# Performance work log

Hardware: AMD Instinct MI355X
Metric: run time of the kernel (lower is better)

Reference implementation:

```python
import jax, jax.numpy as jnp
import numpy as np

E = 32          # n_routed_experts / num_local_experts
H = 1024        # hidden_size
I = 512         # moe_intermediate_size
G = 8           # n_group
TKG = 4         # topk_group
TOPK = 8        # num_experts_per_tok
NSH = 2         # n_shared_experts
SCALE = 2.5     # routed_scaling_factor


def setup_inputs() -> dict:
    key = jax.random.key(0)
    ks = jax.random.split(key, 10)
    s = 0.02
    return {
        "hidden_states": jax.random.normal(ks[0], (2, 1024, H), jnp.float32),
        # router: linear weight [E, H] and e_score_correction_bias [E]
        "gate_w": jax.random.normal(ks[1], (E, H), jnp.float32) * s,
        "gate_bias": jax.random.normal(ks[2], (E,), jnp.float32) * s,
        # routed experts (stacked SwiGLU weights, torch Linear layout [out, in])
        "w_gate": jax.random.normal(ks[3], (E, I, H), jnp.float32) * s,
        "w_up": jax.random.normal(ks[4], (E, I, H), jnp.float32) * s,
        "w_down": jax.random.normal(ks[5], (E, H, I), jnp.float32) * s,
        # shared experts: one MLP with intermediate = I * NSH
        "sh_gate": jax.random.normal(ks[6], (I * NSH, H), jnp.float32) * s,
        "sh_up": jax.random.normal(ks[7], (I * NSH, H), jnp.float32) * s,
        "sh_down": jax.random.normal(ks[8], (H, I * NSH), jnp.float32) * s,
    }


def reference(hidden_states, gate_w, gate_bias, w_gate, w_up, w_down,
              sh_gate, sh_up, sh_down):
    B, S, Hd = hidden_states.shape
    h = hidden_states.reshape(-1, Hd)                      # [T, H]

    # ---- router (DeepseekV3TopkRouter + route_tokens_to_experts) ----
    logits = h.astype(jnp.float32) @ gate_w.T              # [T, E]
    scores = jax.nn.sigmoid(logits)
    sc = scores + gate_bias                                # scores_for_choice
    # group score = sum of top-2 expert scores within each group
    grp = sc.reshape(-1, G, E // G)                        # [T, G, E/G]
    group_scores = jax.lax.top_k(grp, 2)[0].sum(-1)        # [T, G]
    gidx = jax.lax.top_k(group_scores, TKG)[1]             # [T, TKG]
    gmask = jnp.sum(jax.nn.one_hot(gidx, G, dtype=sc.dtype), axis=1)  # [T, G]
    smask = jnp.repeat(gmask, E // G, axis=1)              # [T, E]
    masked = jnp.where(smask > 0, sc, jnp.zeros_like(sc))  # masked_fill(~mask, 0)
    tki = jax.lax.top_k(masked, TOPK)[1]                   # [T, TOPK]
    tkw = jnp.take_along_axis(scores, tki, axis=1)         # gather raw sigmoid scores
    tkw = tkw / (tkw.sum(-1, keepdims=True) + 1e-20)       # norm_topk_prob
    tkw = tkw * SCALE

    # ---- dispatch-compute-combine (experts_forward) ----
    # combine[t, e] = sum_k tkw[t, k] * [tki[t, k] == e]
    combine = (jax.nn.one_hot(tki, E, dtype=tkw.dtype) * tkw[..., None]).sum(1)  # [T, E]
    g = jax.nn.silu(jnp.einsum('th,eih->tei', h, w_gate))  # [T, E, I]
    u = jnp.einsum('th,eih->tei', h, w_up)                 # [T, E, I]
    routed = jnp.einsum('tei,ehi->th', g * u * combine[:, :, None], w_down)  # [T, H]

    # ---- shared experts ----
    sg = jax.nn.silu(h @ sh_gate.T)
    shared = (sg * (h @ sh_up.T)) @ sh_down.T              # [T, H]

    return (routed + shared).reshape(B, S, Hd)
```

## Files before the change

kernel.cpp:

```cpp
#include <hip/hip_runtime.h>
#include <hip/hip_bf16.h>
#include <cstdint>

#define E_ 32
#define H_ 1024
#define I_ 512
#define G_ 8
#define NSH_ 2
#define SCALE_ 2.5f
#define NROUTED (E_ * I_)
#define PADCAP (16384 + E_ * 128)

typedef unsigned short u16;
using bf16x8_t = __attribute__((ext_vector_type(8))) __bf16;
using f32x4_t  = __attribute__((ext_vector_type(4))) float;

__device__ __forceinline__ u16 f2bf(float x) {
  union { float f; uint32_t u; } v; v.f = x;
  uint32_t u = v.u;
  uint32_t r = (u + 0x7fffu + ((u >> 16) & 1u)) >> 16;
  return (u16)r;
}
__device__ __forceinline__ float bf2f(u16 x) {
  union { uint32_t u; float f; } v; v.u = ((uint32_t)x) << 16; return v.f;
}

__device__ __forceinline__ void load_lds16(const void* g, void* l) {
  __builtin_amdgcn_global_load_lds(
      (const __attribute__((address_space(1))) unsigned int*)g,
      (__attribute__((address_space(3))) unsigned int*)l,
      16, 0, 0);
}

#define OFF_BU   16777216L
#define OFF_BD   33554432L
#define OFF_BSHG 50331648L
#define OFF_BSHU 51380224L
#define OFF_BSHD 52428800L
#define WBF_TOT  53477376L

#define W4_WG  4194304L
#define W4_WU  8388608L
#define W4_WD  12582912L
#define W4_SHG 12845056L
#define W4_SHU 13107200L
#define W4_TOT 13369344L
__global__ void prep_kernel(const float* __restrict__ gw, float* __restrict__ gwT,
                            int* __restrict__ counts, int* __restrict__ cursor,
                            int* __restrict__ qheads,
                            int* __restrict__ tok_list, float* __restrict__ wt_list,
                            const float* __restrict__ wg, const float* __restrict__ wu,
                            const float* __restrict__ wd, const float* __restrict__ shg,
                            const float* __restrict__ shu, const float* __restrict__ shd,
                            u16* __restrict__ wbf) {
  long i0 = (long)blockIdx.x * blockDim.x + threadIdx.x;
  if (i0 < H_ * E_) {
    int k = (int)(i0 >> 5), e = (int)(i0 & 31);
    gwT[i0] = gw[(long)e * H_ + k];
  }
  if (i0 < PADCAP) { tok_list[i0] = 0; wt_list[i0] = 0.f; }
  if (i0 < E_) { counts[i0] = 0; cursor[i0] = 0; }
  if (i0 < 2) qheads[i0] = 0;

  long stride = (long)gridDim.x * blockDim.x;
  for (long i = i0; i < W4_TOT; i += stride) {
    const float* s; long off; long dofs;
    if (i < W4_WG)       { s = wg;  off = i;            dofs = off * 4; }
    else if (i < W4_WU)  { s = wu;  off = i - W4_WG;    dofs = OFF_BU + off * 4; }
    else if (i < W4_WD)  { s = wd;  off = i - W4_WU;    dofs = OFF_BD + off * 4; }
    else if (i < W4_SHG) { s = shg; off = i - W4_WD;    dofs = OFF_BSHG + off * 4; }
    else if (i < W4_SHU) { s = shu; off = i - W4_SHG;   dofs = OFF_BSHU + off * 4; }
    else                 { s = shd; off = i - W4_SHU;   dofs = OFF_BSHD + off * 4; }
    float4 v = ((const float4*)s)[off];
    ushort4 o;
    o.x = f2bf(v.x); o.y = f2bf(v.y); o.z = f2bf(v.z); o.w = f2bf(v.w);
    *(ushort4*)(wbf + dofs) = o;
  }
}

__global__ __launch_bounds__(256) void logits_kernel(
    const float* __restrict__ h, const float* __restrict__ gwT,
    float* __restrict__ lpart,
    u16* __restrict__ hbf, int T) {
  __shared__ float shh[64][128];
  __shared__ float shw[128][E_];
  const int tid = threadIdx.x;
  const int t0 = blockIdx.x * 64;
  const int k0 = blockIdx.y * 128;
  #pragma unroll
  for (int i = 0; i < 8; ++i) {
    int c = tid + 256 * i;
    int row = c >> 5, col = c & 31;
    float4 v = *(const float4*)(h + (size_t)(t0 + row) * H_ + k0 + col * 4);
    *(float4*)(&shh[row][col * 4]) = v;
    ushort4 o;
    o.x = f2bf(v.x); o.y = f2bf(v.y); o.z = f2bf(v.z); o.w = f2bf(v.w);
    *(ushort4*)(hbf + (size_t)(t0 + row) * H_ + k0 + col * 4) = o;
  }
  #pragma unroll
  for (int i = 0; i < 4; ++i) {
    int c = tid + 256 * i;
    int row = c >> 3, col = c & 7;
    *(float4*)(&shw[row][col * 4]) =
        *(const float4*)(gwT + (size_t)(k0 + row) * E_ + col * 4);
  }
  __syncthreads();
  const int e = tid & 31;
  const int tb = (tid >> 5) * 8;
  float acc[8] = {0.f, 0.f, 0.f, 0.f, 0.f, 0.f, 0.f, 0.f};
  #pragma unroll 4
  for (int k = 0; k < 128; ++k) {
    float wv = shw[k][e];
    #pragma unroll
    for (int j = 0; j < 8; ++j) acc[j] += shh[tb + j][k] * wv;
  }
  #pragma unroll
  for (int j = 0; j < 8; ++j)
    lpart[((size_t)blockIdx.y * T + (t0 + tb + j)) * E_ + e] = acc[j];
}

__global__ __launch_bounds__(256) void topk_kernel(
    const float* __restrict__ lpart, const float* __restrict__ gb,
    int* __restrict__ idx8, float* __restrict__ wt8, int* __restrict__ counts,
    int T) {
  const int tid = threadIdx.x;
  const int l = tid & 63, wid = tid >> 6;
  const int e = l & 31, half = l >> 5;
  const int t = blockIdx.x * 8 + wid * 2 + half;

  float lg = 0.f;
  #pragma unroll
  for (int s = 0; s < 8; ++s) lg += lpart[((size_t)s * T + t) * E_ + e];
  float score = 1.f / (1.f + __expf(-lg));
  float sc = score + gb[e];

  float x1 = __shfl_xor(sc, 1);
  float x2 = __shfl_xor(sc, 2);
  float x3 = __shfl_xor(sc, 3);
  float hi1 = fmaxf(sc, x1), lo1 = fminf(sc, x1);
  float hi2 = fmaxf(x2, x3), lo2 = fminf(x2, x3);
  float m1 = fmaxf(hi1, hi2);
  float m2 = (hi1 >= hi2) ? fmaxf(lo1, hi2) : fmaxf(lo2, hi1);
  float gs = m1 + m2;

  float ga[8];
  #pragma unroll
  for (int g = 0; g < 8; ++g) ga[g] = __shfl(gs, (half << 5) + g * 4);
  unsigned gm = 0;
  #pragma unroll
  for (int r = 0; r < 4; ++r) {
    float bv = -1e30f; int bi = 0;
    #pragma unroll
    for (int g = 0; g < 8; ++g)
      if (!((gm >> g) & 1u) && ga[g] > bv) { bv = ga[g]; bi = g; }
    gm |= 1u << bi;
  }
  float msk = ((gm >> (e >> 2)) & 1u) ? sc : 0.f;

  float wsum = 0.f, myw = 0.f;
  int myi = 0;
  #pragma unroll
  for (int r = 0; r < 8; ++r) {
    float av = msk; int ai = e;
    #pragma unroll
    for (int m = 16; m; m >>= 1) {
      float ov = __shfl_xor(av, m);
      int oi = __shfl_xor(ai, m);
      if (ov > av || (ov == av && oi < ai)) { av = ov; ai = oi; }
    }
    float wscore = __shfl(score, (half << 5) + ai);
    wsum += wscore;
    if (e == r) { myi = ai; myw = wscore; }
    if (e == ai) msk = 0.f;
  }
  float inv = SCALE_ / (wsum + 1e-20f);
  if (e < 8) {
    idx8[(size_t)t * 8 + e] = myi;
    wt8[(size_t)t * 8 + e] = myw * inv;
    atomicAdd(&counts[myi], 1);
  }
}

__global__ void fill_kernel(const int* __restrict__ idx8, const float* __restrict__ wt8,
                            const int* __restrict__ counts, int* __restrict__ cursor,
                            int* __restrict__ tok_list, float* __restrict__ wt_list,
                            int* __restrict__ pair_pos, int npair) {
  int i = blockIdx.x * blockDim.x + threadIdx.x;
  if (i >= npair) return;
  int e = idx8[i];
  int offz = 0;
  for (int k = 0; k < E_; ++k) {
    if (k == e) break;
    offz += ((counts[k] + 127) >> 7) << 7;
  }
  int p = atomicAdd(&cursor[e], 1);
  int slot = offz + p;
  tok_list[slot] = i >> 3;
  wt_list[slot] = wt8[i];
  pair_pos[i] = slot;
}

__global__ __launch_bounds__(256, 3) void p1_kernel(
    const u16* __restrict__ hbf,
    const u16* __restrict__ wbf,
    const int* __restrict__ counts,
    const int* __restrict__ tok_list, const float* __restrict__ wt_list,
    int* __restrict__ qheads,
    u16* __restrict__ gu,
    u16* __restrict__ gu_sh,
    int T) {
  __shared__ u16 lsA[3][128 * 32];
  __shared__ u16 lsB0[3][64 * 32];
  __shared__ u16 lsB1[3][64 * 32];
  __shared__ int s_tok[128];
  __shared__ float s_wt[128];
  __shared__ int s_off[E_], s_ntt[E_];
  __shared__ int s_tot, s_tile;

  const int tid = threadIdx.x;
  if (tid == 0) {
    int run = 0, tot = 0;
    for (int e = 0; e < E_; ++e) {
      s_off[e] = run;
      int nt = (counts[e] + 127) >> 7;
      s_ntt[e] = nt;
      run += nt << 7;
      tot += nt * 8;
    }
    s_tot = tot + (T / 128) * 16;
  }

  const int w = tid >> 6, l = tid & 63;
  const int wr = w >> 1, wc = w & 1;
  const int lr = l & 15, lh = l >> 4;
  const int rdblk = (lh ^ ((lr >> 1) & 3)) << 3;

  const int rA0 = tid >> 2,          cb0 = tid & 3, sc0 = cb0 ^ ((rA0 >> 1) & 3);
  const int rA1 = (tid + 256) >> 2,  sc1 = cb0 ^ ((rA1 >> 1) & 3);

  for (;;) {
    __syncthreads();
    if (tid == 0) s_tile = atomicAdd(&qheads[0], 1);
    __syncthreads();
    int q = s_tile;
    if (q >= s_tot) break;

    int z = 0, rem = q;
    for (; z < E_; ++z) { int t = s_ntt[z] * 8; if (rem < t) break; rem -= t; }
    const bool sh_e = (z == E_);
    int tt, nb;
    if (sh_e) { nb = rem >> 4; tt = rem & 15; }
    else      { int nt = s_ntt[z]; nb = rem / nt; tt = rem - nb * nt; }
    const int off = sh_e ? 0 : s_off[z];

    if (tid < 128) {
      if (sh_e) { s_tok[tid] = tt * 128 + tid; s_wt[tid] = 1.0f; }
      else {
        int slot = off + tt * 128 + tid;
        s_tok[tid] = tok_list[slot];
        s_wt[tid] = wt_list[slot];
      }
    }
    __syncthreads();

    const u16* Bg = sh_e ? (wbf + OFF_BSHG + (size_t)(nb * 64) * H_)
                         : (wbf + ((size_t)z * I_ + nb * 64) * H_);
    const u16* Bu = sh_e ? (wbf + OFF_BSHU + (size_t)(nb * 64) * H_)
                         : (wbf + OFF_BU + ((size_t)z * I_ + nb * 64) * H_);
    const u16* A0p = hbf + (size_t)s_tok[rA0] * H_ + sc0 * 8;
    const u16* A1p = hbf + (size_t)s_tok[rA1] * H_ + sc1 * 8;
    const u16* Bgp = Bg + (size_t)rA0 * H_ + sc0 * 8;
    const u16* Bup = Bu + (size_t)rA0 * H_ + sc0 * 8;

    f32x4_t acc0[4][2], acc1[4][2];
    #pragma unroll
    for (int m = 0; m < 4; ++m)
      #pragma unroll
      for (int n = 0; n < 2; ++n) {
        acc0[m][n] = (f32x4_t){0.f, 0.f, 0.f, 0.f};
        acc1[m][n] = (f32x4_t){0.f, 0.f, 0.f, 0.f};
      }

    auto stage = [&](int b, int ks) {
      int k0 = ks * 32;
      load_lds16(A0p + k0, (char*)&lsA[b][0] + tid * 16);
      load_lds16(A1p + k0, (char*)&lsA[b][0] + (tid + 256) * 16);
      load_lds16(Bgp + k0, (char*)&lsB0[b][0] + tid * 16);
      load_lds16(Bup + k0, (char*)&lsB1[b][0] + tid * 16);
    };
    auto compute = [&](int b) {
      bf16x8_t af[4], b0f[2], b1f[2];
      #pragma unroll
      for (int m = 0; m < 4; ++m)
        af[m] = *(const bf16x8_t*)(&lsA[b][0] + (wr * 64 + m * 16 + lr) * 32 + rdblk);
      #pragma unroll
      for (int n = 0; n < 2; ++n) {
        b0f[n] = *(const bf16x8_t*)(&lsB0[b][0] + (wc * 32 + n * 16 + lr) * 32 + rdblk);
        b1f[n] = *(const bf16x8_t*)(&lsB1[b][0] + (wc * 32 + n * 16 + lr) * 32 + rdblk);
      }
      #pragma unroll
      for (int m = 0; m < 4; ++m)
        #pragma unroll
        for (int n = 0; n < 2; ++n) {
          acc0[m][n] = __builtin_amdgcn_mfma_f32_16x16x32_bf16(af[m], b0f[n], acc0[m][n], 0, 0, 0);
          acc1[m][n] = __builtin_amdgcn_mfma_f32_16x16x32_bf16(af[m], b1f[n], acc1[m][n], 0, 0, 0);
        }
    };

    stage(0, 0);
    stage(1, 1);
    int b0 = 0, b1 = 1, b2 = 2;
    #pragma unroll 1
    for (int s = 0; s < 31; ++s) {
      asm volatile("s_waitcnt vmcnt(4)" ::: "memory");
      __builtin_amdgcn_s_barrier();
      compute(b0);
      if (s < 30) stage(b2, s + 2);
      int tb = b0; b0 = b1; b1 = b2; b2 = tb;
    }
    asm volatile("s_waitcnt vmcnt(0)" ::: "memory");
    __builtin_amdgcn_s_barrier();
    compute(b0);

    const int ldo = sh_e ? (I_ * NSH_) : I_;
    u16* outp = sh_e ? (gu_sh + (size_t)(tt * 128) * ldo + nb * 64)
                     : (gu + (size_t)(off + tt * 128) * ldo + nb * 64);
    #pragma unroll
    for (int m = 0; m < 4; ++m) {
      #pragma unroll
      for (int n = 0; n < 2; ++n) {
        int col = wc * 32 + n * 16 + lr;
        #pragma unroll
        for (int j = 0; j < 4; ++j) {
          int trow = wr * 64 + m * 16 + lh * 4 + j;
          float gv = acc0[m][n][j], uv = acc1[m][n][j];
          float sv = gv / (1.f + __expf(-gv));
          outp[(size_t)trow * ldo + col] = f2bf(sv * uv * s_wt[trow]);
        }
      }
    }
  }
}

__global__ __launch_bounds__(256, 3) void p2_kernel(
    const u16* __restrict__ gu, const u16* __restrict__ gu_sh,
    const u16* __restrict__ wbf,
    const int* __restrict__ counts,
    int* __restrict__ qheads,
    u16* __restrict__ part,
    u16* __restrict__ part_sh,
    int T) {
  __shared__ u16 lsA[3][128 * 32];
  __shared__ u16 lsB[3][128 * 32];
  __shared__ int s_off[E_], s_ntt[E_];
  __shared__ int s_tot, s_tile;

  const int tid = threadIdx.x;
  if (tid == 0) {
    int run = 0, tot = 0;
    for (int e = 0; e < E_; ++e) {
      s_off[e] = run;
      int nt = (counts[e] + 127) >> 7;
      s_ntt[e] = nt;
      run += nt << 7;
      tot += nt * 8;
    }
    s_tot = tot + (T / 128) * 8;
  }

  const int w = tid >> 6, l = tid & 63;
  const int wr = w >> 1, wc = w & 1;
  const int lr = l & 15, lh = l >> 4;
  const int rdblk = (lh ^ ((lr >> 1) & 3)) << 3;

  const int c0 = tid, c1 = tid + 256;
  const int row0 = c0 >> 2, cb0 = c0 & 3, scb0 = cb0 ^ ((row0 >> 1) & 3);
  const int row1 = c1 >> 2, cb1 = c1 & 3, scb1 = cb1 ^ ((row1 >> 1) & 3);

  for (;;) {
    __syncthreads();
    if (tid == 0) s_tile = atomicAdd(&qheads[1], 1);
    __syncthreads();
    int q = s_tile;
    if (q >= s_tot) break;

    int z = 0, rem = q;
    for (; z < E_; ++z) { int t = s_ntt[z] * 8; if (rem < t) break; rem -= t; }
    const bool sh_e = (z == E_);
    int tt = rem >> 3, nb = rem & 7;

    const int K = sh_e ? (I_ * NSH_) : I_;
    const int NT = K / 32;
    const u16* Ab = sh_e ? (gu_sh + (size_t)(tt * 128) * K)
                         : (gu + (size_t)(s_off[z] + tt * 128) * K);
    const u16* Bb = sh_e ? (wbf + OFF_BSHD + (size_t)(nb * 128) * K)
                         : (wbf + OFF_BD + (size_t)z * H_ * I_ + (size_t)(nb * 128) * K);
    u16* outp = sh_e ? (part_sh + (size_t)(tt * 128) * H_ + nb * 128)
                     : (part + (size_t)(s_off[z] + tt * 128) * H_ + nb * 128);

    f32x4_t acc[4][4];
    #pragma unroll
    for (int m = 0; m < 4; ++m)
      #pragma unroll
      for (int n = 0; n < 4; ++n) acc[m][n] = (f32x4_t){0.f, 0.f, 0.f, 0.f};

    auto stage = [&](int b, int ks) {
      int k0 = ks * 32;
      load_lds16(Ab + (size_t)row0 * K + k0 + scb0 * 8, (char*)&lsA[b][0] + c0 * 16);
      load_lds16(Ab + (size_t)row1 * K + k0 + scb1 * 8, (char*)&lsA[b][0] + c1 * 16);
      load_lds16(Bb + (size_t)row0 * K + k0 + scb0 * 8, (char*)&lsB[b][0] + c0 * 16);
      load_lds16(Bb + (size_t)row1 * K + k0 + scb1 * 8, (char*)&lsB[b][0] + c1 * 16);
    };
    auto compute = [&](int b) {
      bf16x8_t af[4], bf[4];
      #pragma unroll
      for (int m = 0; m < 4; ++m)
        af[m] = *(const bf16x8_t*)(&lsA[b][0] + (wr * 64 + m * 16 + lr) * 32 + rdblk);
      #pragma unroll
      for (int n = 0; n < 4; ++n)
        bf[n] = *(const bf16x8_t*)(&lsB[b][0] + (wc * 64 + n * 16 + lr) * 32 + rdblk);
      #pragma unroll
      for (int m = 0; m < 4; ++m)
        #pragma unroll
        for (int n = 0; n < 4; ++n)
          acc[m][n] = __builtin_amdgcn_mfma_f32_16x16x32_bf16(af[m], bf[n], acc[m][n], 0, 0, 0);
    };

    stage(0, 0);
    stage(1, 1);
    int b0 = 0, b1 = 1, b2 = 2;
    #pragma unroll 1
    for (int s = 0; s < NT - 1; ++s) {
      asm volatile("s_waitcnt vmcnt(4)" ::: "memory");
      __builtin_amdgcn_s_barrier();
      compute(b0);
      if (s + 2 < NT) stage(b2, s + 2);
      int tb = b0; b0 = b1; b1 = b2; b2 = tb;
    }
    asm volatile("s_waitcnt vmcnt(0)" ::: "memory");
    __builtin_amdgcn_s_barrier();
    compute(b0);

    u16* eb = &lsA[0][0];
    #pragma unroll
    for (int half = 0; half < 2; ++half) {
      __syncthreads();
      if (wr == half) {
        #pragma unroll
        for (int m = 0; m < 4; ++m) {
          #pragma unroll
          for (int n = 0; n < 4; ++n) {
            int col = wc * 64 + n * 16 + lr;
            #pragma unroll
            for (int j = 0; j < 4; ++j)
              eb[(m * 16 + lh * 4 + j) * 128 + col] = f2bf(acc[m][n][j]);
          }
        }
      }
      __syncthreads();
      #pragma unroll
      for (int i = 0; i < 8; ++i) {
        int c = tid + 256 * i;
        int row = c >> 5, col4 = c & 31;
        *(ushort4*)(outp + (size_t)(half * 64 + row) * H_ + col4 * 4) =
            *(const ushort4*)(eb + row * 128 + col4 * 4);
      }
    }
  }
}

__global__ void combine_kernel(const u16* __restrict__ part, const u16* __restrict__ part_sh,
                               const int* __restrict__ pair_pos, float* __restrict__ out) {
  int t = blockIdx.x;
  int h = threadIdx.x * 4;
  int pp[8];
  #pragma unroll
  for (int s = 0; s < 8; ++s) pp[s] = pair_pos[(long)t * 8 + s];
  ushort4 v = *(const ushort4*)(part_sh + (size_t)t * H_ + h);
  float a0 = bf2f(v.x), a1 = bf2f(v.y), a2 = bf2f(v.z), a3 = bf2f(v.w);
  #pragma unroll
  for (int s = 0; s < 8; ++s) {
    ushort4 u = *(const ushort4*)(part + (size_t)pp[s] * H_ + h);
    a0 += bf2f(u.x); a1 += bf2f(u.y); a2 += bf2f(u.z); a3 += bf2f(u.w);
  }
  float4 o = {a0, a1, a2, a3};
  *(float4*)(out + (size_t)t * H_ + h) = o;
}

extern "C" void kernel_launch(void* const* d_in, const int* in_sizes, int n_in,
                              void* d_out, int out_size, void* d_ws, size_t ws_size,
                              hipStream_t stream) {
  const float* hs  = (const float*)d_in[0];
  const float* gw  = (const float*)d_in[1];
  const float* gb  = (const float*)d_in[2];
  const float* wg  = (const float*)d_in[3];
  const float* wu  = (const float*)d_in[4];
  const float* wd  = (const float*)d_in[5];
  const float* shg = (const float*)d_in[6];
  const float* shu = (const float*)d_in[7];
  const float* shd = (const float*)d_in[8];
  float* out = (float*)d_out;

  const int T = in_sizes[0] / H_;

  char* ws = (char*)d_ws;
  size_t off = 0;
  auto alloc = [&](size_t bytes) {
    char* p = ws + off;
    off += (bytes + 255) & ~(size_t)255;
    return p;
  };
  int*   counts   = (int*)alloc(E_ * 4);
  int*   cursor   = (int*)alloc(E_ * 4);
  int*   qheads   = (int*)alloc(2 * 4);
  int*   idx8     = (int*)alloc((size_t)T * 8 * 4);
  float* wt8      = (float*)alloc((size_t)T * 8 * 4);
  int*   pair_pos = (int*)alloc((size_t)T * 8 * 4);
  int*   tok_list = (int*)alloc(PADCAP * 4);
  float* wt_list  = (float*)alloc(PADCAP * 4);
  float* gwT      = (float*)alloc((size_t)H_ * E_ * 4);
  float* lpart    = (float*)alloc((size_t)8 * T * E_ * 4);
  u16* hbf     = (u16*)alloc((size_t)T * H_ * 2);
  u16* wbf     = (u16*)alloc((size_t)WBF_TOT * 2);
  u16* gu      = (u16*)alloc((size_t)PADCAP * I_ * 2);
  u16* gu_sh   = (u16*)alloc((size_t)T * I_ * NSH_ * 2);
  u16* part    = (u16*)alloc((size_t)PADCAP * H_ * 2);
  u16* part_sh = (u16*)alloc((size_t)T * H_ * 2);
  if (off > ws_size) return;

  hipLaunchKernelGGL(prep_kernel, dim3(4096), dim3(256), 0, stream,
                     gw, gwT, counts, cursor, qheads, tok_list, wt_list,
                     wg, wu, wd, shg, shu, shd, wbf);

  hipLaunchKernelGGL(logits_kernel, dim3(T / 64, 8), dim3(256), 0, stream,
                     hs, gwT, lpart, hbf, T);

  hipLaunchKernelGGL(topk_kernel, dim3(T / 8), dim3(256), 0, stream,
                     lpart, gb, idx8, wt8, counts, T);

  hipLaunchKernelGGL(fill_kernel, dim3((T * 8 + 255) / 256), dim3(256), 0, stream,
                     idx8, wt8, counts, cursor, tok_list, wt_list, pair_pos, T * 8);

  hipLaunchKernelGGL(p1_kernel, dim3(768), dim3(256), 0, stream,
                     hbf, wbf, counts, tok_list, wt_list, qheads, gu, gu_sh, T);

  hipLaunchKernelGGL(p2_kernel, dim3(768), dim3(256), 0, stream,
                     gu, gu_sh, wbf, counts, qheads, part, part_sh, T);

  hipLaunchKernelGGL(combine_kernel, dim3(T), dim3(256), 0, stream,
                     part, part_sh, pair_pos, out);
}
```

Measured before the change: 283.3 us.

## Move down-projection weight conversion into p1 tail and raise MFMA priority

```diff
diff --git a/kernel.cpp b/kernel.cpp
--- a/kernel.cpp
+++ b/kernel.cpp
@@ -39,19 +39,12 @@
 #define OFF_BSHD 52428800L
 #define WBF_TOT  53477376L
 
-#define W4_WG  4194304L
-#define W4_WU  8388608L
-#define W4_WD  12582912L
-#define W4_SHG 12845056L
-#define W4_SHU 13107200L
-#define W4_TOT 13369344L
 __global__ void prep_kernel(const float* __restrict__ gw, float* __restrict__ gwT,
                             int* __restrict__ counts, int* __restrict__ cursor,
                             int* __restrict__ qheads,
                             int* __restrict__ tok_list, float* __restrict__ wt_list,
                             const float* __restrict__ wg, const float* __restrict__ wu,
-                            const float* __restrict__ wd, const float* __restrict__ shg,
-                            const float* __restrict__ shu, const float* __restrict__ shd,
+                            const float* __restrict__ shg, const float* __restrict__ shu,
                             u16* __restrict__ wbf) {
   long i0 = (long)blockIdx.x * blockDim.x + threadIdx.x;
   if (i0 < H_ * E_) {
@@ -63,14 +56,12 @@
   if (i0 < 2) qheads[i0] = 0;
 
   long stride = (long)gridDim.x * blockDim.x;
-  for (long i = i0; i < W4_TOT; i += stride) {
+  for (long i = i0; i < 8912896L; i += stride) {
     const float* s; long off; long dofs;
-    if (i < W4_WG)       { s = wg;  off = i;            dofs = off * 4; }
-    else if (i < W4_WU)  { s = wu;  off = i - W4_WG;    dofs = OFF_BU + off * 4; }
-    else if (i < W4_WD)  { s = wd;  off = i - W4_WU;    dofs = OFF_BD + off * 4; }
-    else if (i < W4_SHG) { s = shg; off = i - W4_WD;    dofs = OFF_BSHG + off * 4; }
-    else if (i < W4_SHU) { s = shu; off = i - W4_SHG;   dofs = OFF_BSHU + off * 4; }
-    else                 { s = shd; off = i - W4_SHU;   dofs = OFF_BSHD + off * 4; }
+    if (i < 4194304L)      { s = wg;  off = i;            dofs = off * 4; }
+    else if (i < 8388608L) { s = wu;  off = i - 4194304L; dofs = OFF_BU + off * 4; }
+    else if (i < 8650752L) { s = shg; off = i - 8388608L; dofs = OFF_BSHG + off * 4; }
+    else                   { s = shu; off = i - 8650752L; dofs = OFF_BSHU + off * 4; }
     float4 v = ((const float4*)s)[off];
     ushort4 o;
     o.x = f2bf(v.x); o.y = f2bf(v.y); o.z = f2bf(v.z); o.w = f2bf(v.w);
@@ -206,6 +197,8 @@
     const int* __restrict__ counts,
     const int* __restrict__ tok_list, const float* __restrict__ wt_list,
     int* __restrict__ qheads,
+    const float* __restrict__ wd, const float* __restrict__ shd,
+    u16* wbf_mut,
     u16* __restrict__ gu,
     u16* __restrict__ gu_sh,
     int T) {
@@ -298,6 +291,7 @@
         b0f[n] = *(const bf16x8_t*)(&lsB0[b][0] + (wc * 32 + n * 16 + lr) * 32 + rdblk);
         b1f[n] = *(const bf16x8_t*)(&lsB1[b][0] + (wc * 32 + n * 16 + lr) * 32 + rdblk);
       }
+      __builtin_amdgcn_s_setprio(1);
       #pragma unroll
       for (int m = 0; m < 4; ++m)
         #pragma unroll
@@ -305,6 +299,7 @@
           acc0[m][n] = __builtin_amdgcn_mfma_f32_16x16x32_bf16(af[m], b0f[n], acc0[m][n], 0, 0, 0);
           acc1[m][n] = __builtin_amdgcn_mfma_f32_16x16x32_bf16(af[m], b1f[n], acc1[m][n], 0, 0, 0);
         }
+      __builtin_amdgcn_s_setprio(0);
     };
 
     stage(0, 0);
@@ -339,6 +334,16 @@
         }
       }
     }
+  }
+
+  const long WD4 = 4194304L, TOT4 = 4456448L;
+  for (long i = (long)blockIdx.x * 256 + tid; i < TOT4; i += (long)gridDim.x * 256) {
+    float4 v; long dofs;
+    if (i < WD4) { v = ((const float4*)wd)[i]; dofs = OFF_BD + i * 4; }
+    else { v = ((const float4*)shd)[i - WD4]; dofs = OFF_BSHD + (i - WD4) * 4; }
+    ushort4 o;
+    o.x = f2bf(v.x); o.y = f2bf(v.y); o.z = f2bf(v.z); o.w = f2bf(v.w);
+    *(ushort4*)(wbf_mut + dofs) = o;
   }
 }
 
@@ -419,11 +424,13 @@
       #pragma unroll
       for (int n = 0; n < 4; ++n)
         bf[n] = *(const bf16x8_t*)(&lsB[b][0] + (wc * 64 + n * 16 + lr) * 32 + rdblk);
+      __builtin_amdgcn_s_setprio(1);
       #pragma unroll
       for (int m = 0; m < 4; ++m)
         #pragma unroll
         for (int n = 0; n < 4; ++n)
           acc[m][n] = __builtin_amdgcn_mfma_f32_16x16x32_bf16(af[m], bf[n], acc[m][n], 0, 0, 0);
+      __builtin_amdgcn_s_setprio(0);
     };
 
     stage(0, 0);
@@ -530,7 +537,7 @@
 
   hipLaunchKernelGGL(prep_kernel, dim3(4096), dim3(256), 0, stream,
                      gw, gwT, counts, cursor, qheads, tok_list, wt_list,
-                     wg, wu, wd, shg, shu, shd, wbf);
+                     wg, wu, shg, shu, wbf);
 
   hipLaunchKernelGGL(logits_kernel, dim3(T / 64, 8), dim3(256), 0, stream,
                      hs, gwT, lpart, hbf, T);
@@ -542,7 +549,8 @@
                      idx8, wt8, counts, cursor, tok_list, wt_list, pair_pos, T * 8);
 
   hipLaunchKernelGGL(p1_kernel, dim3(768), dim3(256), 0, stream,
-                     hbf, wbf, counts, tok_list, wt_list, qheads, gu, gu_sh, T);
+                     hbf, wbf, counts, tok_list, wt_list, qheads,
+                     wd, shd, wbf, gu, gu_sh, T);
 
   hipLaunchKernelGGL(p2_kernel, dim3(768), dim3(256), 0, stream,
                      gu, gu_sh, wbf, counts, qheads, part, part_sh, T);
```

After: 285.1 us. Within noise of the previous version (+0.7%).

## Merge weight prep and router logits into one kernel; store p2 output directly

Applied to the files above, without the earlier changes.

```diff
diff --git a/kernel.cpp b/kernel.cpp
--- a/kernel.cpp
+++ b/kernel.cpp
@@ -45,78 +45,72 @@
 #define W4_SHG 12845056L
 #define W4_SHU 13107200L
 #define W4_TOT 13369344L
-__global__ void prep_kernel(const float* __restrict__ gw, float* __restrict__ gwT,
-                            int* __restrict__ counts, int* __restrict__ cursor,
-                            int* __restrict__ qheads,
-                            int* __restrict__ tok_list, float* __restrict__ wt_list,
-                            const float* __restrict__ wg, const float* __restrict__ wu,
-                            const float* __restrict__ wd, const float* __restrict__ shg,
-                            const float* __restrict__ shu, const float* __restrict__ shd,
-                            u16* __restrict__ wbf) {
-  long i0 = (long)blockIdx.x * blockDim.x + threadIdx.x;
-  if (i0 < H_ * E_) {
-    int k = (int)(i0 >> 5), e = (int)(i0 & 31);
-    gwT[i0] = gw[(long)e * H_ + k];
-  }
-  if (i0 < PADCAP) { tok_list[i0] = 0; wt_list[i0] = 0.f; }
-  if (i0 < E_) { counts[i0] = 0; cursor[i0] = 0; }
-  if (i0 < 2) qheads[i0] = 0;
-
-  long stride = (long)gridDim.x * blockDim.x;
-  for (long i = i0; i < W4_TOT; i += stride) {
-    const float* s; long off; long dofs;
-    if (i < W4_WG)       { s = wg;  off = i;            dofs = off * 4; }
-    else if (i < W4_WU)  { s = wu;  off = i - W4_WG;    dofs = OFF_BU + off * 4; }
-    else if (i < W4_WD)  { s = wd;  off = i - W4_WU;    dofs = OFF_BD + off * 4; }
-    else if (i < W4_SHG) { s = shg; off = i - W4_WD;    dofs = OFF_BSHG + off * 4; }
-    else if (i < W4_SHU) { s = shu; off = i - W4_SHG;   dofs = OFF_BSHU + off * 4; }
-    else                 { s = shd; off = i - W4_SHU;   dofs = OFF_BSHD + off * 4; }
-    float4 v = ((const float4*)s)[off];
-    ushort4 o;
-    o.x = f2bf(v.x); o.y = f2bf(v.y); o.z = f2bf(v.z); o.w = f2bf(v.w);
-    *(ushort4*)(wbf + dofs) = o;
-  }
-}
-
-__global__ __launch_bounds__(256) void logits_kernel(
-    const float* __restrict__ h, const float* __restrict__ gwT,
+
+__global__ __launch_bounds__(256) void prep_logits_kernel(
+    const float* __restrict__ h, const float* __restrict__ gw,
     float* __restrict__ lpart,
-    u16* __restrict__ hbf, int T) {
-  __shared__ float shh[64][128];
-  __shared__ float shw[128][E_];
+    u16* __restrict__ hbf,
+    int* __restrict__ counts, int* __restrict__ cursor, int* __restrict__ qheads,
+    int* __restrict__ tok_list, float* __restrict__ wt_list,
+    const float* __restrict__ wg, const float* __restrict__ wu,
+    const float* __restrict__ wd, const float* __restrict__ shg,
+    const float* __restrict__ shu, const float* __restrict__ shd,
+    u16* __restrict__ wbf, int T) {
   const int tid = threadIdx.x;
-  const int t0 = blockIdx.x * 64;
-  const int k0 = blockIdx.y * 128;
-  #pragma unroll
-  for (int i = 0; i < 8; ++i) {
-    int c = tid + 256 * i;
-    int row = c >> 5, col = c & 31;
-    float4 v = *(const float4*)(h + (size_t)(t0 + row) * H_ + k0 + col * 4);
-    *(float4*)(&shh[row][col * 4]) = v;
-    ushort4 o;
-    o.x = f2bf(v.x); o.y = f2bf(v.y); o.z = f2bf(v.z); o.w = f2bf(v.w);
-    *(ushort4*)(hbf + (size_t)(t0 + row) * H_ + k0 + col * 4) = o;
-  }
-  #pragma unroll
-  for (int i = 0; i < 4; ++i) {
-    int c = tid + 256 * i;
-    int row = c >> 3, col = c & 7;
-    *(float4*)(&shw[row][col * 4]) =
-        *(const float4*)(gwT + (size_t)(k0 + row) * E_ + col * 4);
-  }
-  __syncthreads();
-  const int e = tid & 31;
-  const int tb = (tid >> 5) * 8;
-  float acc[8] = {0.f, 0.f, 0.f, 0.f, 0.f, 0.f, 0.f, 0.f};
-  #pragma unroll 4
-  for (int k = 0; k < 128; ++k) {
-    float wv = shw[k][e];
-    #pragma unroll
-    for (int j = 0; j < 8; ++j) acc[j] += shh[tb + j][k] * wv;
-  }
-  #pragma unroll
-  for (int j = 0; j < 8; ++j)
-    lpart[((size_t)blockIdx.y * T + (t0 + tb + j)) * E_ + e] = acc[j];
+  if (blockIdx.x < 256) {
+    __shared__ float shh[64][128];
+    __shared__ float shw[128][E_];
+    const int t0 = (blockIdx.x & 31) * 64;
+    const int k0 = (blockIdx.x >> 5) * 128;
+    #pragma unroll
+    for (int i = 0; i < 8; ++i) {
+      int c = tid + 256 * i;
+      int row = c >> 5, col = c & 31;
+      float4 v = *(const float4*)(h + (size_t)(t0 + row) * H_ + k0 + col * 4);
+      *(float4*)(&shh[row][col * 4]) = v;
+      ushort4 o;
+      o.x = f2bf(v.x); o.y = f2bf(v.y); o.z = f2bf(v.z); o.w = f2bf(v.w);
+      *(ushort4*)(hbf + (size_t)(t0 + row) * H_ + k0 + col * 4) = o;
+    }
+    #pragma unroll
+    for (int i = 0; i < 16; ++i) {
+      int c = tid + 256 * i;
+      int e = c >> 7, row = c & 127;
+      shw[row][e] = gw[(size_t)e * H_ + k0 + row];
+    }
+    __syncthreads();
+    const int e = tid & 31;
+    const int tb = (tid >> 5) * 8;
+    float acc[8] = {0.f, 0.f, 0.f, 0.f, 0.f, 0.f, 0.f, 0.f};
+    #pragma unroll 4
+    for (int k = 0; k < 128; ++k) {
+      float wv = shw[k][e];
+      #pragma unroll
+      for (int j = 0; j < 8; ++j) acc[j] += shh[tb + j][k] * wv;
+    }
+    #pragma unroll
+    for (int j = 0; j < 8; ++j)
+      lpart[((size_t)(blockIdx.x >> 5) * T + (t0 + tb + j)) * E_ + e] = acc[j];
+  } else {
+    long i0 = (long)(blockIdx.x - 256) * 256 + tid;
+    if (i0 < PADCAP) { tok_list[i0] = 0; wt_list[i0] = 0.f; }
+    if (i0 < E_) { counts[i0] = 0; cursor[i0] = 0; }
+    if (i0 < 2) qheads[i0] = 0;
+    const long stride = 2048L * 256;
+    for (long i = i0; i < W4_TOT; i += stride) {
+      const float* s; long off; long dofs;
+      if (i < W4_WG)       { s = wg;  off = i;            dofs = off * 4; }
+      else if (i < W4_WU)  { s = wu;  off = i - W4_WG;    dofs = OFF_BU + off * 4; }
+      else if (i < W4_WD)  { s = wd;  off = i - W4_WU;    dofs = OFF_BD + off * 4; }
+      else if (i < W4_SHG) { s = shg; off = i - W4_WD;    dofs = OFF_BSHG + off * 4; }
+      else if (i < W4_SHU) { s = shu; off = i - W4_SHG;   dofs = OFF_BSHU + off * 4; }
+      else                 { s = shd; off = i - W4_SHU;   dofs = OFF_BSHD + off * 4; }
+      float4 v = ((const float4*)s)[off];
+      ushort4 o;
+      o.x = f2bf(v.x); o.y = f2bf(v.y); o.z = f2bf(v.z); o.w = f2bf(v.w);
+      *(ushort4*)(wbf + dofs) = o;
+    }
+  }
 }
 
 __global__ __launch_bounds__(256) void topk_kernel(
@@ -441,29 +435,16 @@
     __builtin_amdgcn_s_barrier();
     compute(b0);
 
-    u16* eb = &lsA[0][0];
-    #pragma unroll
-    for (int half = 0; half < 2; ++half) {
-      __syncthreads();
-      if (wr == half) {
+    #pragma unroll
+    for (int m = 0; m < 4; ++m) {
+      #pragma unroll
+      for (int n = 0; n < 4; ++n) {
+        int col = wc * 64 + n * 16 + lr;
         #pragma unroll
-        for (int m = 0; m < 4; ++m) {
-          #pragma unroll
-          for (int n = 0; n < 4; ++n) {
-            int col = wc * 64 + n * 16 + lr;
-            #pragma unroll
-            for (int j = 0; j < 4; ++j)
-              eb[(m * 16 + lh * 4 + j) * 128 + col] = f2bf(acc[m][n][j]);
-          }
+        for (int j = 0; j < 4; ++j) {
+          int trow = wr * 64 + m * 16 + lh * 4 + j;
+          outp[(size_t)trow * H_ + col] = f2bf(acc[m][n][j]);
         }
-      }
-      __syncthreads();
-      #pragma unroll
-      for (int i = 0; i < 8; ++i) {
-        int c = tid + 256 * i;
-        int row = c >> 5, col4 = c & 31;
-        *(ushort4*)(outp + (size_t)(half * 64 + row) * H_ + col4 * 4) =
-            *(const ushort4*)(eb + row * 128 + col4 * 4);
       }
     }
   }
@@ -518,7 +499,6 @@
   int*   pair_pos = (int*)alloc((size_t)T * 8 * 4);
   int*   tok_list = (int*)alloc(PADCAP * 4);
   float* wt_list  = (float*)alloc(PADCAP * 4);
-  float* gwT      = (float*)alloc((size_t)H_ * E_ * 4);
   float* lpart    = (float*)alloc((size_t)8 * T * E_ * 4);
   u16* hbf     = (u16*)alloc((size_t)T * H_ * 2);
   u16* wbf     = (u16*)alloc((size_t)WBF_TOT * 2);
@@ -528,12 +508,9 @@
   u16* part_sh = (u16*)alloc((size_t)T * H_ * 2);
   if (off > ws_size) return;
 
-  hipLaunchKernelGGL(prep_kernel, dim3(4096), dim3(256), 0, stream,
-                     gw, gwT, counts, cursor, qheads, tok_list, wt_list,
-                     wg, wu, wd, shg, shu, shd, wbf);
-
-  hipLaunchKernelGGL(logits_kernel, dim3(T / 64, 8), dim3(256), 0, stream,
-                     hs, gwT, lpart, hbf, T);
+  hipLaunchKernelGGL(prep_logits_kernel, dim3(2304), dim3(256), 0, stream,
+                     hs, gw, lpart, hbf, counts, cursor, qheads,
+                     tok_list, wt_list, wg, wu, wd, shg, shu, shd, wbf, T);
 
   hipLaunchKernelGGL(topk_kernel, dim3(T / 8), dim3(256), 0, stream,
                      lpart, gb, idx8, wt8, counts, T);
```

Measured after the change: 273.6 us. 1.04x faster.
